# Kernel optimization log

Measured on AMD Instinct MI355X. Metric: run time of the kernel, lower is better.

## Reference

```python
import jax, jax.numpy as jnp
from jax import lax
import numpy as np

L, D, DM, E, DH, K, V, B, S = 4, 512, 128, 2, 128, 5, 50257, 2, 1024
EPS = 1e-6


def rmsnorm(x, w):
    return w * x * jax.lax.rsqrt(jnp.mean(x * x, axis=-1, keepdims=True) + EPS)


def rope(x):
    b, s, d = x.shape
    h = d // 2
    inv = 1.0 / (10000.0 ** (jnp.arange(h, dtype=jnp.float32) / h))
    freqs = jnp.arange(s, dtype=jnp.float32)[:, None] * inv[None, :]  # [S, h]
    emb = jnp.concatenate([freqs, freqs], axis=-1)  # [S, D]
    cos, sin = jnp.cos(emb)[None], jnp.sin(emb)[None]
    x1, x2 = x[..., :h], x[..., h:]
    rot = jnp.concatenate([-x2, x1], axis=-1)
    return x * cos + rot * sin


def causal_dwconv(x, w, b, dil):
    # x: [B,S,D]; w: [D,K] depthwise kernel; left-pad (K-1)*dil => causal.
    xc = jnp.transpose(x, (0, 2, 1))  # [B,D,S]
    k = w[:, None, :]  # [D,1,K]
    pad = (w.shape[-1] - 1) * dil
    y = lax.conv_general_dilated(xc, k, window_strides=(1,), padding=[(pad, 0)],
                                 rhs_dilation=(dil,),
                                 dimension_numbers=('NCH', 'OIH', 'NCH'),
                                 feature_group_count=x.shape[-1])
    return jnp.transpose(y, (0, 2, 1)) + b


def recurrence(x, win, bin_, wf, bf, wu, bu, wo, bo):
    # StructuredStateRecurrence: gated scan over time with memory dim DM.
    b_, s_, d_ = x.shape
    mu = jax.nn.silu(x @ win.T + bin_)            # [B,S,DM] silu(memory_proj_in)
    fx = x @ wf[:, :d_].T + bf                    # x-part of forget gate
    ux = x @ wu[:, :d_].T + bu                    # x-part of update gate
    ox = x @ wo[:, :d_].T + bo                    # x-part of output gate
    wfm, wum, wom = wf[:, d_:], wu[:, d_:], wo[:, d_:]

    def step(m, inp):
        fx_t, ux_t, mu_t, ox_t, x_t = inp
        f = jax.nn.sigmoid(fx_t + m @ wfm.T)
        u = jax.nn.sigmoid(ux_t + m @ wum.T)
        m = f * m + u * mu_t
        out = x_t + ox_t + m @ wom.T
        return m, out

    m0 = jnp.zeros((b_, DM), x.dtype)
    tr = lambda a: jnp.transpose(a, (1, 0, 2))
    m_final, ys = lax.scan(step, m0, (tr(fx), tr(ux), tr(mu), tr(ox), tr(x)))
    return jnp.transpose(ys, (1, 0, 2)), m_final


def setup_inputs() -> dict:
    key = jax.random.key(0)
    ks = iter(jax.random.split(key, 40))
    p = lambda shape, s=0.02: jax.random.normal(next(ks), shape, jnp.float32) * s
    return dict(
        tokens=jax.random.randint(next(ks), (B, S), 0, V),
        embed=p((V, D)),
        norm_w=jnp.ones((L, D)),
        dw_w=p((L, D, K), 0.1), dw_b=jnp.zeros((L, D)),
        pw_w=p((L, D, D)), pw_b=jnp.zeros((L, D)),
        rin_w=p((L, DM, D)), rin_b=jnp.zeros((L, DM)),
        rf_w=p((L, DM, D + DM)), rf_b=jnp.ones((L, DM)),
        ru_w=p((L, DM, D + DM)), ru_b=jnp.zeros((L, DM)),
        ro_w=p((L, D, D + DM)), ro_b=jnp.zeros((L, D)),
        rt_w=p((L, E, D)), rt_b=jnp.zeros((L, E)),
        e1_w=p((L, E, D, D)), e1_b=jnp.zeros((L, E, D)),
        e2_w=p((L, E, D, D)), e2_b=jnp.zeros((L, E, D)),
        fn_w=jnp.ones((L, D)),
        fd_w=p((L, DH, D)), fd_b=jnp.zeros((L, DH)),
        fu_w=p((L, D, DH)), fu_b=jnp.zeros((L, D)),
        final_norm_w=jnp.ones((D,)),
    )


def reference(tokens, embed, norm_w, dw_w, dw_b, pw_w, pw_b,
              rin_w, rin_b, rf_w, rf_b, ru_w, ru_b, ro_w, ro_b,
              rt_w, rt_b, e1_w, e1_b, e2_w, e2_b, fn_w,
              fd_w, fd_b, fu_w, fu_b, final_norm_w):
    dils = [max(1, int(np.exp(i * np.log(8) / L))) for i in range(L)]  # [1,1,2,4]
    x = embed[tokens]            # [B,S,D] token embedding
    x = rope(x)                  # rotary positional embedding (applied to full dim)
    for i in range(L):
        residual = x
        xn = rmsnorm(x, norm_w[i])
        # depthwise causal dilated conv + 1x1 pointwise conv
        xc = causal_dwconv(xn, dw_w[i], dw_b[i], dils[i])
        xc = xc @ pw_w[i].T + pw_b[i]
        # gated recurrent memory scan
        xr, _ = recurrence(xn, rin_w[i], rin_b[i], rf_w[i], rf_b[i],
                           ru_w[i], ru_b[i], ro_w[i], ro_b[i])
        h = xc + xr
        # EnhancedGatedFusion: softmax router over 2 dense experts
        r = jax.nn.softmax(h @ rt_w[i].T + rt_b[i], axis=-1)          # [B,S,E]
        hh = jax.nn.silu(jnp.einsum('bsd,eod->bseo', h, e1_w[i]) + e1_b[i])
        eo = jnp.einsum('bseo,epo->bsep', hh, e2_w[i]) + e2_b[i]      # [B,S,E,D]
        h = rmsnorm(h + jnp.einsum('bse,bsep->bsp', r, eo), fn_w[i])
        # LowRankFF: down -> GELU(exact) -> up
        h = h + (jax.nn.gelu(h @ fd_w[i].T + fd_b[i], approximate=False) @ fu_w[i].T + fu_b[i])
        x = h + residual
    x = rmsnorm(x, final_norm_w)
    logits = x @ embed.T          # tied output projection
    return logits
```

## Files before the change

### kernel.cpp

```cpp
#include <hip/hip_runtime.h>
#include <hip/hip_bf16.h>

#define Bsz 2
#define Ssz 1024
#define Dsz 512
#define DMs 128
#define Vsz 50257
#define ROWS (Bsz*Ssz)

typedef __attribute__((ext_vector_type(8))) short short8;
typedef __attribute__((ext_vector_type(4))) float f32x4;
typedef __attribute__((ext_vector_type(8))) int int8v;
typedef __attribute__((ext_vector_type(4))) int int4v;

#define DEV static __device__ __forceinline__

DEV unsigned short f2bf(float f){
  unsigned int u = __float_as_uint(f);
  unsigned int r = ((u >> 16) & 1u) + 0x7fffu;
  return (unsigned short)((u + r) >> 16);
}

__global__ __launch_bounds__(256) void k_embed_rope(
    const int* __restrict__ tokens, const float* __restrict__ embed, float* __restrict__ x)
{
  int row = blockIdx.x;
  int s = row & (Ssz-1);
  int t = threadIdx.x;
  int tok = tokens[row];
  const float* e = embed + (size_t)tok * Dsz;
  float e1 = e[t], e2 = e[t + 256];
  float inv = powf(10000.f, -(float)t * (1.f/256.f));
  float fr = (float)s * inv;
  float sn, cs;
  sincosf(fr, &sn, &cs);
  float* o = x + (size_t)row * Dsz;
  o[t]       = e1 * cs - e2 * sn;
  o[t + 256] = e2 * cs + e1 * sn;
}

__global__ __launch_bounds__(256) void k_rmsnorm(
    const float* __restrict__ a, const float* __restrict__ w, float* __restrict__ out)
{
  int row = blockIdx.x; int t = threadIdx.x;
  size_t base = (size_t)row * Dsz;
  float v0 = a[base + t];
  float v1 = a[base + t + 256];
  float ss = v0*v0 + v1*v1;
  #pragma unroll
  for (int off = 32; off > 0; off >>= 1) ss += __shfl_down(ss, off);
  __shared__ float sred[4];
  __shared__ float sscale;
  int wid = t >> 6, lane = t & 63;
  if (lane == 0) sred[wid] = ss;
  __syncthreads();
  if (t == 0) {
    float tot = sred[0] + sred[1] + sred[2] + sred[3];
    sscale = rsqrtf(tot * (1.f/Dsz) + 1e-6f);
  }
  __syncthreads();
  float sc = sscale;
  out[base + t]       = w[t]       * v0 * sc;
  out[base + t + 256] = w[t + 256] * v1 * sc;
}

__global__ __launch_bounds__(256) void k_rmsnorm_b16(
    const float* __restrict__ a, const float* __restrict__ w, unsigned short* __restrict__ out)
{
  int row = blockIdx.x; int t = threadIdx.x;
  size_t base = (size_t)row * Dsz;
  float v0 = a[base + t];
  float v1 = a[base + t + 256];
  float ss = v0*v0 + v1*v1;
  #pragma unroll
  for (int off = 32; off > 0; off >>= 1) ss += __shfl_down(ss, off);
  __shared__ float sred[4];
  __shared__ float sscale;
  int wid = t >> 6, lane = t & 63;
  if (lane == 0) sred[wid] = ss;
  __syncthreads();
  if (t == 0) {
    float tot = sred[0] + sred[1] + sred[2] + sred[3];
    sscale = rsqrtf(tot * (1.f/Dsz) + 1e-6f);
  }
  __syncthreads();
  float sc = sscale;
  out[base + t]       = f2bf(w[t]       * v0 * sc);
  out[base + t + 256] = f2bf(w[t + 256] * v1 * sc);
}

__global__ __launch_bounds__(256) void k_combine_norm(
    const float* __restrict__ h, const float* __restrict__ e0,
    const float* __restrict__ e1, const float* __restrict__ rg,
    const float* __restrict__ w, float* __restrict__ out)
{
  int row = blockIdx.x; int t = threadIdx.x;
  size_t base = (size_t)row * Dsz;
  float r0 = rg[row*2], r1 = rg[row*2+1];
  float v0 = h[base + t]       + r0*e0[base + t]       + r1*e1[base + t];
  float v1 = h[base + t + 256] + r0*e0[base + t + 256] + r1*e1[base + t + 256];
  float ss = v0*v0 + v1*v1;
  #pragma unroll
  for (int off = 32; off > 0; off >>= 1) ss += __shfl_down(ss, off);
  __shared__ float sred[4];
  __shared__ float sscale;
  int wid = t >> 6, lane = t & 63;
  if (lane == 0) sred[wid] = ss;
  __syncthreads();
  if (t == 0) {
    float tot = sred[0] + sred[1] + sred[2] + sred[3];
    sscale = rsqrtf(tot * (1.f/Dsz) + 1e-6f);
  }
  __syncthreads();
  float sc = sscale;
  out[base + t]       = w[t]       * v0 * sc;
  out[base + t + 256] = w[t + 256] * v1 * sc;
}

__global__ __launch_bounds__(256) void k_dwconv(
    const float* __restrict__ xn, const float* __restrict__ w,
    const float* __restrict__ bias, float* __restrict__ out, int dil)
{
  int row = blockIdx.x;
  int b = row >> 10, s = row & (Ssz-1);
  int t = threadIdx.x;
  #pragma unroll
  for (int dd = 0; dd < 2; ++dd) {
    int d = t + dd*256;
    float acc = bias[d];
    #pragma unroll
    for (int j = 0; j < 5; ++j) {
      int sp = s - (4 - j) * dil;
      if (sp >= 0) acc += w[d*5 + j] * xn[((size_t)(b*Ssz + sp))*Dsz + d];
    }
    out[(size_t)row*Dsz + d] = acc;
  }
}

__global__ __launch_bounds__(256) void k_gemm128(
    const float* __restrict__ A, int lda,
    const float* __restrict__ B, int ldb,
    const float* __restrict__ bias,
    float* __restrict__ C, int ldc,
    int M, int N, int K)
{
  __shared__ __align__(16) unsigned short As[128][40];
  __shared__ __align__(16) unsigned short Bs[128][40];
  int t = threadIdx.x;
  int m0 = blockIdx.y * 128;
  int n0 = blockIdx.x * 128;
  int wid = t >> 6, lane = t & 63;
  int wr = wid >> 1, wc = wid & 1;
  f32x4 acc[4][4] = {};
  int tr = t >> 3;
  int tc = (t & 7) * 4;

  for (int k0 = 0; k0 < K; k0 += 32) {
    #pragma unroll
    for (int rr = 0; rr < 128; rr += 32) {
      int row = rr + tr;
      float4 av = *reinterpret_cast<const float4*>(A + (size_t)(m0 + row)*lda + k0 + tc);
      ushort4 ap; ap.x = f2bf(av.x); ap.y = f2bf(av.y); ap.z = f2bf(av.z); ap.w = f2bf(av.w);
      *reinterpret_cast<ushort4*>(&As[row][tc]) = ap;
      int bn = n0 + row;
      float4 bv = make_float4(0.f, 0.f, 0.f, 0.f);
      if (bn < N) bv = *reinterpret_cast<const float4*>(B + (size_t)bn*ldb + k0 + tc);
      ushort4 bp; bp.x = f2bf(bv.x); bp.y = f2bf(bv.y); bp.z = f2bf(bv.z); bp.w = f2bf(bv.w);
      *reinterpret_cast<ushort4*>(&Bs[row][tc]) = bp;
    }
    __syncthreads();
    int kc = (lane >> 4) * 8;
    int ra = lane & 15;
    short8 af[4], bf_[4];
    #pragma unroll
    for (int mt = 0; mt < 4; ++mt)
      af[mt] = *reinterpret_cast<const short8*>(&As[wr*64 + mt*16 + ra][kc]);
    #pragma unroll
    for (int nt = 0; nt < 4; ++nt)
      bf_[nt] = *reinterpret_cast<const short8*>(&Bs[wc*64 + nt*16 + ra][kc]);
    #pragma unroll
    for (int mt = 0; mt < 4; ++mt)
      #pragma unroll
      for (int nt = 0; nt < 4; ++nt)
        acc[mt][nt] = __builtin_amdgcn_mfma_f32_16x16x32_bf16(af[mt], bf_[nt], acc[mt][nt], 0, 0, 0);
    __syncthreads();
  }

  #pragma unroll
  for (int mt = 0; mt < 4; ++mt) {
    #pragma unroll
    for (int nt = 0; nt < 4; ++nt) {
      int n = n0 + wc*64 + nt*16 + (lane & 15);
      if (n >= N) continue;
      float bv = bias ? bias[n] : 0.f;
      #pragma unroll
      for (int j = 0; j < 4; ++j) {
        int m = m0 + wr*64 + mt*16 + (lane >> 4)*4 + j;
        C[(size_t)m*ldc + n] = acc[mt][nt][j] + bv;
      }
    }
  }
}

template<int OP, int NADD>
DEV void gemm64_body(unsigned short (*As)[40], unsigned short (*Bs)[40],
                     const float* __restrict__ A, int lda,
                     const float* __restrict__ B, int ldb,
                     const float* __restrict__ bias,
                     float* __restrict__ C, int ldc,
                     int K, int m0, int n0, int t,
                     const float* __restrict__ add1,
                     const float* __restrict__ add2,
                     const float* __restrict__ add3)
{
  int lane = t & 63;
  int wid = t >> 6;
  int wr = wid >> 1, wc = wid & 1;
  f32x4 acc[2][2] = {};
  int srow = t >> 2;
  int scb  = (t & 3) * 8;

  const float* apg = A + (size_t)(m0 + srow)*lda + scb;
  const float* bpg = B + (size_t)(n0 + srow)*ldb + scb;

  for (int k0 = 0; k0 < K; k0 += 32) {
    float4 a0 = *reinterpret_cast<const float4*>(apg + k0);
    float4 a1 = *reinterpret_cast<const float4*>(apg + k0 + 4);
    float4 b0 = *reinterpret_cast<const float4*>(bpg + k0);
    float4 b1 = *reinterpret_cast<const float4*>(bpg + k0 + 4);
    short8 av, bv;
    av[0]=f2bf(a0.x); av[1]=f2bf(a0.y); av[2]=f2bf(a0.z); av[3]=f2bf(a0.w);
    av[4]=f2bf(a1.x); av[5]=f2bf(a1.y); av[6]=f2bf(a1.z); av[7]=f2bf(a1.w);
    bv[0]=f2bf(b0.x); bv[1]=f2bf(b0.y); bv[2]=f2bf(b0.z); bv[3]=f2bf(b0.w);
    bv[4]=f2bf(b1.x); bv[5]=f2bf(b1.y); bv[6]=f2bf(b1.z); bv[7]=f2bf(b1.w);
    *reinterpret_cast<short8*>(&As[srow][scb]) = av;
    *reinterpret_cast<short8*>(&Bs[srow][scb]) = bv;
    __syncthreads();
    int kc = (lane >> 4) * 8;
    int ra = lane & 15;
    short8 af[2], bf_[2];
    #pragma unroll
    for (int mt = 0; mt < 2; ++mt)
      af[mt] = *reinterpret_cast<const short8*>(&As[wr*32 + mt*16 + ra][kc]);
    #pragma unroll
    for (int nt = 0; nt < 2; ++nt)
      bf_[nt] = *reinterpret_cast<const short8*>(&Bs[wc*32 + nt*16 + ra][kc]);
    #pragma unroll
    for (int mt = 0; mt < 2; ++mt)
      #pragma unroll
      for (int nt = 0; nt < 2; ++nt)
        acc[mt][nt] = __builtin_amdgcn_mfma_f32_16x16x32_bf16(af[mt], bf_[nt], acc[mt][nt], 0, 0, 0);
    __syncthreads();
  }

  #pragma unroll
  for (int mt = 0; mt < 2; ++mt) {
    #pragma unroll
    for (int nt = 0; nt < 2; ++nt) {
      int n = n0 + wc*32 + nt*16 + (lane & 15);
      float bv = bias ? bias[n] : 0.f;
      #pragma unroll
      for (int j = 0; j < 4; ++j) {
        int m = m0 + wr*32 + mt*16 + (lane >> 4)*4 + j;
        float v = acc[mt][nt][j] + bv;
        if (OP == 1) v = v / (1.f + expf(-v));
        else if (OP == 2) v = 0.5f * v * (1.f + erff(v * 0.70710678118f));
        size_t idx = (size_t)m*ldc + n;
        if (NADD >= 1) v += add1[idx];
        if (NADD >= 2) v += add2[idx];
        if (NADD >= 3) v += add3[idx];
        C[idx] = v;
      }
    }
  }
}

template<int OP, int NADD>
__global__ __launch_bounds__(256) void k_gemm64(
    const float* __restrict__ A, int lda,
    const float* __restrict__ B, int ldb,
    const float* __restrict__ bias,
    float* __restrict__ C, int ldc, int K,
    const float* add1, const float* add2, const float* add3)
{
  __shared__ __align__(16) unsigned short As[64][40];
  __shared__ __align__(16) unsigned short Bs[64][40];
  gemm64_body<OP,NADD>(As, Bs, A, lda, B, ldb, bias, C, ldc, K,
                       blockIdx.y*64, blockIdx.x*64, threadIdx.x, add1, add2, add3);
}

__global__ __launch_bounds__(256) void k_proj3(
    const float* __restrict__ xn,
    const float* __restrict__ rin_w, const float* __restrict__ rin_b,
    const float* __restrict__ rf_w,  const float* __restrict__ rf_b,
    const float* __restrict__ ru_w,  const float* __restrict__ ru_b,
    float* __restrict__ mu, float* __restrict__ fx, float* __restrict__ ux)
{
  __shared__ __align__(16) unsigned short As[64][40];
  __shared__ __align__(16) unsigned short Bs[64][40];
  int which = blockIdx.x >> 1;
  int n0 = (blockIdx.x & 1) * 64;
  int m0 = blockIdx.y * 64;
  if (which == 0)
    gemm64_body<1,0>(As, Bs, xn, Dsz, rin_w, Dsz, rin_b, mu, DMs, Dsz, m0, n0, threadIdx.x, nullptr, nullptr, nullptr);
  else if (which == 1)
    gemm64_body<0,0>(As, Bs, xn, Dsz, rf_w, 640, rf_b, fx, DMs, Dsz, m0, n0, threadIdx.x, nullptr, nullptr, nullptr);
  else
    gemm64_body<0,0>(As, Bs, xn, Dsz, ru_w, 640, ru_b, ux, DMs, Dsz, m0, n0, threadIdx.x, nullptr, nullptr, nullptr);
}

template<int OP>
__global__ __launch_bounds__(256) void k_expair(
    const float* __restrict__ A0, const float* __restrict__ A1, int lda,
    const float* __restrict__ B0, const float* __restrict__ B1, int ldb,
    const float* __restrict__ bias0, const float* __restrict__ bias1,
    float* __restrict__ C0, float* __restrict__ C1, int ldc, int K)
{
  __shared__ __align__(16) unsigned short As[64][40];
  __shared__ __align__(16) unsigned short Bs[64][40];
  int e = blockIdx.x >> 3;
  int n0 = (blockIdx.x & 7) * 64;
  gemm64_body<OP,0>(As, Bs, e ? A1 : A0, lda, e ? B1 : B0, ldb,
                    e ? bias1 : bias0, e ? C1 : C0, ldc, K,
                    blockIdx.y*64, n0, threadIdx.x, nullptr, nullptr, nullptr);
}

__global__ __launch_bounds__(256) void k_f2b(
    const float* __restrict__ in, unsigned short* __restrict__ o, int n8)
{
  int stride = gridDim.x * 256;
  for (int i = blockIdx.x*256 + threadIdx.x; i < n8; i += stride) {
    float4 a = reinterpret_cast<const float4*>(in)[i*2];
    float4 b = reinterpret_cast<const float4*>(in)[i*2+1];
    short8 v;
    v[0]=f2bf(a.x); v[1]=f2bf(a.y); v[2]=f2bf(a.z); v[3]=f2bf(a.w);
    v[4]=f2bf(b.x); v[5]=f2bf(b.y); v[6]=f2bf(b.z); v[7]=f2bf(b.w);
    *reinterpret_cast<short8*>(o + (size_t)i*8) = v;
  }
}

__global__ __launch_bounds__(256) void k_gemm_logits(
    const unsigned short* __restrict__ A, const unsigned short* __restrict__ B,
    float* __restrict__ C, int M, int N, int K)
{
  __shared__ __align__(16) unsigned short As[128][40];
  __shared__ __align__(16) unsigned short Bs[128][40];
  int t = threadIdx.x;
  int lin = blockIdx.x + blockIdx.y * 16;
  int swz = (lin & 7) * 786 + (lin >> 3);
  int m0 = (swz & 15) * 128;
  int n0 = (swz >> 4) * 128;
  int wid = t >> 6, lane = t & 63;
  int wr = wid >> 1, wc = wid & 1;
  f32x4 acc[4][4] = {};
  int srow = t >> 1;
  int scb  = (t & 1) * 16;

  const unsigned short* ap = A + (size_t)(m0 + srow)*K + scb;
  int bn = n0 + srow; if (bn >= N) bn = N - 1;
  const unsigned short* bp = B + (size_t)bn*K + scb;

  for (int k0 = 0; k0 < K; k0 += 32) {
    short8 a0 = *reinterpret_cast<const short8*>(ap + k0);
    short8 a1 = *reinterpret_cast<const short8*>(ap + k0 + 8);
    short8 b0 = *reinterpret_cast<const short8*>(bp + k0);
    short8 b1 = *reinterpret_cast<const short8*>(bp + k0 + 8);
    *reinterpret_cast<short8*>(&As[srow][scb])     = a0;
    *reinterpret_cast<short8*>(&As[srow][scb + 8]) = a1;
    *reinterpret_cast<short8*>(&Bs[srow][scb])     = b0;
    *reinterpret_cast<short8*>(&Bs[srow][scb + 8]) = b1;
    __syncthreads();
    int kc = (lane >> 4) * 8;
    int ra = lane & 15;
    short8 af[4], bf_[4];
    #pragma unroll
    for (int mt = 0; mt < 4; ++mt)
      af[mt] = *reinterpret_cast<const short8*>(&As[wr*64 + mt*16 + ra][kc]);
    #pragma unroll
    for (int nt = 0; nt < 4; ++nt)
      bf_[nt] = *reinterpret_cast<const short8*>(&Bs[wc*64 + nt*16 + ra][kc]);
    #pragma unroll
    for (int mt = 0; mt < 4; ++mt)
      #pragma unroll
      for (int nt = 0; nt < 4; ++nt)
        acc[mt][nt] = __builtin_amdgcn_mfma_f32_16x16x32_bf16(af[mt], bf_[nt], acc[mt][nt], 0, 0, 0);
    __syncthreads();
  }

  #pragma unroll
  for (int mt = 0; mt < 4; ++mt) {
    #pragma unroll
    for (int nt = 0; nt < 4; ++nt) {
      int n = n0 + wc*64 + nt*16 + (lane & 15);
      if (n >= N) continue;
      #pragma unroll
      for (int j = 0; j < 4; ++j) {
        int m = m0 + wr*64 + mt*16 + (lane >> 4)*4 + j;
        C[(size_t)m*N + n] = acc[mt][nt][j];
      }
    }
  }
}

__global__ __launch_bounds__(256, 2) void k_scan_fused(
    const float* __restrict__ rf_w, const float* __restrict__ ru_w,
    const float* __restrict__ fx, const float* __restrict__ ux,
    const float* __restrict__ mu, float* __restrict__ Mout,
    const float* __restrict__ g1A, const float* __restrict__ g1B, int g1ldb,
    const float* __restrict__ g1bias, float* __restrict__ g1C,
    const float* __restrict__ g2A, const float* __restrict__ g2B, int g2ldb,
    const float* __restrict__ g2bias, float* __restrict__ g2C)
{
  __shared__ __align__(16) unsigned short As[64][40];
  __shared__ __align__(16) unsigned short Bs[64][40];
  __shared__ __align__(16) unsigned char mf8[2][DMs];

  if (blockIdx.x >= 2) {
    int bid = blockIdx.x - 2;
    int which = bid >> 8;
    int idx = bid & 255;
    int n0 = (idx & 7) * 64;
    int m0 = (idx >> 3) * 64;
    if (which == 0)
      gemm64_body<0,0>(As, Bs, g1A, Dsz, g1B, g1ldb, g1bias, g1C, Dsz, Dsz, m0, n0, threadIdx.x, nullptr, nullptr, nullptr);
    else
      gemm64_body<0,0>(As, Bs, g2A, Dsz, g2B, g2ldb, g2bias, g2C, Dsz, Dsz, m0, n0, threadIdx.x, nullptr, nullptr, nullptr);
    return;
  }

  __builtin_amdgcn_s_setprio(1);

  int b = blockIdx.x;
  int t = threadIdx.x;
  int l = t & 63;
  int w = t >> 6;
  int g = l >> 4;
  int i16 = l & 15;

  int8v w8[4];
  #pragma unroll
  for (int rt = 0; rt < 4; ++rt) {
    const float* src = (rt < 2 ? rf_w : ru_w) + (size_t)(w*32 + (rt&1)*16 + i16)*640 + 512 + g*32;
    int8v v;
    #pragma unroll
    for (int bq = 0; bq < 8; ++bq) {
      float4 f4 = *reinterpret_cast<const float4*>(src + bq*4);
      int rr = 0;
      rr = __builtin_amdgcn_cvt_pk_fp8_f32(f4.x, f4.y, rr, false);
      rr = __builtin_amdgcn_cvt_pk_fp8_f32(f4.z, f4.w, rr, true);
      v[bq] = rr;
    }
    w8[rt] = v;
  }

  if (t < DMs) mf8[0][t] = 0;

  bool writer = (i16 & 4) == 0;
  int rho = ((i16 >> 3) << 4) + (g << 2) + (i16 & 3);
  int r = w*32 + rho;
  bool jb0 = (i16 & 1), jb1 = (i16 & 2), ab = (i16 & 8);

  const float* fxp = fx + (size_t)b*Ssz*DMs + r;
  const float* uxp = ux + (size_t)b*Ssz*DMs + r;
  const float* mup = mu + (size_t)b*Ssz*DMs + r;
  float* mo = Mout + (size_t)b*Ssz*DMs + r;
  float mreg = 0.f, fxv = 0.f, uxv = 0.f, muv = 0.f;
  __syncthreads();
  if (writer) { fxv = fxp[0]; uxv = uxp[0]; muv = mup[0]; }

  const int SC = 0x7F7F7F7F;
  int cur = 0;
  for (int step = 0; step < Ssz; ++step) {
    int4v blo = *reinterpret_cast<const int4v*>(&mf8[cur][g*32]);
    int4v bhi = *reinterpret_cast<const int4v*>(&mf8[cur][g*32 + 16]);
    int8v bm;
    bm[0]=blo[0]; bm[1]=blo[1]; bm[2]=blo[2]; bm[3]=blo[3];
    bm[4]=bhi[0]; bm[5]=bhi[1]; bm[6]=bhi[2]; bm[7]=bhi[3];

    f32x4 zero = {0.f, 0.f, 0.f, 0.f};
    f32x4 a0 = __builtin_amdgcn_mfma_scale_f32_16x16x128_f8f6f4(w8[0], bm, zero, 0, 0, 0, SC, 0, SC);
    f32x4 a1 = __builtin_amdgcn_mfma_scale_f32_16x16x128_f8f6f4(w8[1], bm, zero, 0, 0, 0, SC, 0, SC);
    f32x4 a2 = __builtin_amdgcn_mfma_scale_f32_16x16x128_f8f6f4(w8[2], bm, zero, 0, 0, 0, SC, 0, SC);
    f32x4 a3 = __builtin_amdgcn_mfma_scale_f32_16x16x128_f8f6f4(w8[3], bm, zero, 0, 0, 0, SC, 0, SC);

    float f01 = jb0 ? a0[1] : a0[0];
    float f23 = jb0 ? a0[3] : a0[2];
    float fa0 = jb1 ? f23 : f01;
    float f01b = jb0 ? a1[1] : a1[0];
    float f23b = jb0 ? a1[3] : a1[2];
    float fa1 = jb1 ? f23b : f01b;
    float zf = ab ? fa1 : fa0;
    float u01 = jb0 ? a2[1] : a2[0];
    float u23 = jb0 ? a2[3] : a2[2];
    float ua0 = jb1 ? u23 : u01;
    float u01b = jb0 ? a3[1] : a3[0];
    float u23b = jb0 ? a3[3] : a3[2];
    float ua1 = jb1 ? u23b : u01b;
    float zu = ab ? ua1 : ua0;

    if (writer) {
      float f = __builtin_amdgcn_rcpf(1.f + __expf(-(zf + fxv)));
      float u = __builtin_amdgcn_rcpf(1.f + __expf(-(zu + uxv)));
      float mnew = f*mreg + u*muv;
      mreg = mnew;
      int p8 = __builtin_amdgcn_cvt_pk_fp8_f32(mnew, mnew, 0, false);
      mf8[cur^1][r] = (unsigned char)(p8 & 0xff);
      mo[(size_t)step*DMs] = mnew;
      if (step < Ssz-1) {
        fxv = fxp[(size_t)(step+1)*DMs];
        uxv = uxp[(size_t)(step+1)*DMs];
        muv = mup[(size_t)(step+1)*DMs];
      }
    }
    asm volatile("s_waitcnt lgkmcnt(0)\n\ts_barrier" ::: "memory");
    cur ^= 1;
  }
}

__global__ __launch_bounds__(64) void k_rt_softmax(
    const float* __restrict__ h, const float* __restrict__ rtw,
    const float* __restrict__ rtb, float* __restrict__ rg)
{
  int row = blockIdx.x; int lane = threadIdx.x;
  const float* hp = h + (size_t)row*Dsz;
  float a0 = 0.f, a1 = 0.f;
  #pragma unroll
  for (int k = lane; k < Dsz; k += 64) {
    float hv = hp[k];
    a0 += hv * rtw[k];
    a1 += hv * rtw[Dsz + k];
  }
  #pragma unroll
  for (int off = 32; off > 0; off >>= 1) {
    a0 += __shfl_down(a0, off);
    a1 += __shfl_down(a1, off);
  }
  if (lane == 0) {
    a0 += rtb[0]; a1 += rtb[1];
    float mx = fmaxf(a0, a1);
    float e0 = expf(a0 - mx), e1 = expf(a1 - mx);
    float s = e0 + e1;
    rg[row*2]     = e0 / s;
    rg[row*2 + 1] = e1 / s;
  }
}

extern "C" void kernel_launch(void* const* d_in, const int* in_sizes, int n_in,
                              void* d_out, int out_size, void* d_ws, size_t ws_size,
                              hipStream_t stream)
{
  const int*   tokens = (const int*)  d_in[0];
  const float* embed  = (const float*)d_in[1];
  const float* norm_w = (const float*)d_in[2];
  const float* dw_w   = (const float*)d_in[3];
  const float* dw_b   = (const float*)d_in[4];
  const float* pw_w   = (const float*)d_in[5];
  const float* pw_b   = (const float*)d_in[6];
  const float* rin_w  = (const float*)d_in[7];
  const float* rin_b  = (const float*)d_in[8];
  const float* rf_w   = (const float*)d_in[9];
  const float* rf_b   = (const float*)d_in[10];
  const float* ru_w   = (const float*)d_in[11];
  const float* ru_b   = (const float*)d_in[12];
  const float* ro_w   = (const float*)d_in[13];
  const float* ro_b   = (const float*)d_in[14];
  const float* rt_w   = (const float*)d_in[15];
  const float* rt_b   = (const float*)d_in[16];
  const float* e1_w   = (const float*)d_in[17];
  const float* e1_b   = (const float*)d_in[18];
  const float* e2_w   = (const float*)d_in[19];
  const float* e2_b   = (const float*)d_in[20];
  const float* fn_w   = (const float*)d_in[21];
  const float* fd_w   = (const float*)d_in[22];
  const float* fd_b   = (const float*)d_in[23];
  const float* fu_w   = (const float*)d_in[24];
  const float* fu_b   = (const float*)d_in[25];
  const float* fnorm  = (const float*)d_in[26];
  float* out = (float*)d_out;

  float* ws = (float*)d_ws;
  const size_t M1 = 1u << 20;
  float* x   = ws + 0*M1;
  float* xn  = ws + 1*M1;
  float* b2  = ws + 2*M1;
  float* b3  = ws + 3*M1;
  float* h   = ws + 4*M1;
  float* b5  = ws + 5*M1;
  float* b6  = ws + 6*M1;
  float* mu  = ws + 7*M1;
  float* fx  = ws + 7*M1 + 262144;
  float* ux  = ws + 7*M1 + 2*262144;
  float* Mb  = ws + 7*M1 + 3*262144;
  float* g   = ws + 8*M1;
  float* rg  = ws + 8*M1 + 262144;
  const size_t EMB_ELEMS = (size_t)Vsz * Dsz;
  unsigned short* embb = (unsigned short*)(ws + 9*M1);
  bool big = ws_size >= (size_t)(9*M1*4) + EMB_ELEMS*2 + 1024;

  const int dils[4] = {1, 1, 2, 4};

  k_embed_rope<<<ROWS, 256, 0, stream>>>(tokens, embed, x);

  for (int i = 0; i < 4; ++i) {
    k_rmsnorm<<<ROWS,256,0,stream>>>(x, norm_w + i*Dsz, xn);
    k_dwconv<<<ROWS,256,0,stream>>>(xn, dw_w + i*Dsz*5, dw_b + i*Dsz, b2, dils[i]);
    {
      dim3 gr(6, ROWS/64);
      k_proj3<<<gr,256,0,stream>>>(xn,
          rin_w + (size_t)i*DMs*Dsz, rin_b + i*DMs,
          rf_w  + (size_t)i*DMs*640, rf_b  + i*DMs,
          ru_w  + (size_t)i*DMs*640, ru_b  + i*DMs,
          mu, fx, ux);
    }
    k_scan_fused<<<2 + 512, 256, 0, stream>>>(
        rf_w + (size_t)i*DMs*640, ru_w + (size_t)i*DMs*640, fx, ux, mu, Mb,
        b2, pw_w + (size_t)i*Dsz*Dsz, Dsz, pw_b + i*Dsz, b3,
        xn, ro_w + (size_t)i*Dsz*640, 640, ro_b + i*Dsz, b5);
    {
      dim3 gr(Dsz/64, ROWS/64);
      k_gemm64<0,3><<<gr,256,0,stream>>>(Mb,DMs, ro_w + (size_t)i*Dsz*640 + 512,640, nullptr, h,Dsz, DMs, b3, xn, b5);
    }
    k_rt_softmax<<<ROWS,64,0,stream>>>(h, rt_w + i*2*Dsz, rt_b + i*2, rg);
    {
      dim3 ge(16, ROWS/64);
      k_expair<1><<<ge,256,0,stream>>>(h, h, Dsz,
          e1_w + (size_t)(i*2+0)*Dsz*Dsz, e1_w + (size_t)(i*2+1)*Dsz*Dsz, Dsz,
          e1_b + (i*2+0)*Dsz, e1_b + (i*2+1)*Dsz,
          b2, b5, Dsz, Dsz);
      k_expair<0><<<ge,256,0,stream>>>(b2, b5, Dsz,
          e2_w + (size_t)(i*2+0)*Dsz*Dsz, e2_w + (size_t)(i*2+1)*Dsz*Dsz, Dsz,
          e2_b + (i*2+0)*Dsz, e2_b + (i*2+1)*Dsz,
          b3, b6, Dsz, Dsz);
    }
    k_combine_norm<<<ROWS,256,0,stream>>>(h, b3, b6, rg, fn_w + i*Dsz, xn);
    {
      dim3 g1(DMs/64, ROWS/64), g2(Dsz/64, ROWS/64);
      k_gemm64<2,0><<<g1,256,0,stream>>>(xn,Dsz, fd_w + (size_t)i*DMs*Dsz,Dsz, fd_b + i*DMs, g,DMs, Dsz, nullptr,nullptr,nullptr);
      k_gemm64<0,2><<<g2,256,0,stream>>>(g,DMs, fu_w + (size_t)i*Dsz*DMs,DMs, fu_b + i*Dsz, x,Dsz, DMs, x, xn, nullptr);
    }
  }

  if (big) {
    unsigned short* xnb = (unsigned short*)b3;
    k_rmsnorm_b16<<<ROWS,256,0,stream>>>(x, fnorm, xnb);
    k_f2b<<<2048,256,0,stream>>>(embed, embb, (int)(EMB_ELEMS/8));
    dim3 grid(ROWS/128, (Vsz + 127)/128);
    k_gemm_logits<<<grid,256,0,stream>>>(xnb, embb, out, ROWS, Vsz, Dsz);
  } else {
    k_rmsnorm<<<ROWS,256,0,stream>>>(x, fnorm, xn);
    dim3 grid((Vsz + 127)/128, ROWS/128);
    k_gemm128<<<grid,256,0,stream>>>(xn,Dsz, embed,Dsz, nullptr, out,Vsz, ROWS,Vsz,Dsz);
  }
}
```

Baseline: 2.102 ms.

## Overlap embedding bf16 conversion with scan and load logits tiles via direct-to-LDS

The fp32-to-bf16 conversion of the embedding matrix moves out of its own launch before the logits GEMM and into extra blocks of the first layer's scan kernel. There it can run alongside the latency-bound sequential scan on otherwise idle CUs. The logits GEMM also switches its tile loads to global_load_lds direct-to-LDS transfers with an unpadded 32-wide LDS layout, which removes register staging. The unpadded layout may cause LDS bank conflicts on fragment reads, and the extra blocks may compete with the scan blocks for resources.

Result: slower. 2.150 ms (+2.3%).

```diff
diff --git a/kernel.cpp b/kernel.cpp
--- a/kernel.cpp
+++ b/kernel.cpp
@@ -19,6 +19,12 @@
   unsigned int u = __float_as_uint(f);
   unsigned int r = ((u >> 16) & 1u) + 0x7fffu;
   return (unsigned short)((u + r) >> 16);
+}
+
+DEV void gll16(const unsigned short* g, unsigned short* l) {
+  __builtin_amdgcn_global_load_lds(
+      (const __attribute__((address_space(1))) unsigned int*)(g),
+      (__attribute__((address_space(3))) unsigned int*)(l), 16, 0, 0);
 }
 
 __global__ __launch_bounds__(256) void k_embed_rope(
@@ -343,8 +349,8 @@
     const unsigned short* __restrict__ A, const unsigned short* __restrict__ B,
     float* __restrict__ C, int M, int N, int K)
 {
-  __shared__ __align__(16) unsigned short As[128][40];
-  __shared__ __align__(16) unsigned short Bs[128][40];
+  __shared__ __align__(16) unsigned short As[4096];
+  __shared__ __align__(16) unsigned short Bs[4096];
   int t = threadIdx.x;
   int lin = blockIdx.x + blockIdx.y * 16;
   int swz = (lin & 7) * 786 + (lin >> 3);
@@ -353,32 +359,38 @@
   int wid = t >> 6, lane = t & 63;
   int wr = wid >> 1, wc = wid & 1;
   f32x4 acc[4][4] = {};
-  int srow = t >> 1;
-  int scb  = (t & 1) * 16;
-
-  const unsigned short* ap = A + (size_t)(m0 + srow)*K + scb;
-  int bn = n0 + srow; if (bn >= N) bn = N - 1;
-  const unsigned short* bp = B + (size_t)bn*K + scb;
+
+  int row0 = t >> 2;
+  int kcb  = (t & 3) * 8;
+  int row1 = row0 + 64;
+  const unsigned short* a0p = A + (size_t)(m0 + row0)*K + kcb;
+  const unsigned short* a1p = A + (size_t)(m0 + row1)*K + kcb;
+  int bn0 = n0 + row0; if (bn0 >= N) bn0 = N - 1;
+  int bn1 = n0 + row1; if (bn1 >= N) bn1 = N - 1;
+  const unsigned short* b0p = B + (size_t)bn0*K + kcb;
+  const unsigned short* b1p = B + (size_t)bn1*K + kcb;
+
+  unsigned short* lA0 = As + wid*512;
+  unsigned short* lA1 = As + 2048 + wid*512;
+  unsigned short* lB0 = Bs + wid*512;
+  unsigned short* lB1 = Bs + 2048 + wid*512;
+
+  int kc = (lane >> 4) * 8;
+  int ra = lane & 15;
 
   for (int k0 = 0; k0 < K; k0 += 32) {
-    short8 a0 = *reinterpret_cast<const short8*>(ap + k0);
-    short8 a1 = *reinterpret_cast<const short8*>(ap + k0 + 8);
-    short8 b0 = *reinterpret_cast<const short8*>(bp + k0);
-    short8 b1 = *reinterpret_cast<const short8*>(bp + k0 + 8);
-    *reinterpret_cast<short8*>(&As[srow][scb])     = a0;
-    *reinterpret_cast<short8*>(&As[srow][scb + 8]) = a1;
-    *reinterpret_cast<short8*>(&Bs[srow][scb])     = b0;
-    *reinterpret_cast<short8*>(&Bs[srow][scb + 8]) = b1;
+    gll16(a0p + k0, lA0);
+    gll16(a1p + k0, lA1);
+    gll16(b0p + k0, lB0);
+    gll16(b1p + k0, lB1);
     __syncthreads();
-    int kc = (lane >> 4) * 8;
-    int ra = lane & 15;
     short8 af[4], bf_[4];
     #pragma unroll
     for (int mt = 0; mt < 4; ++mt)
-      af[mt] = *reinterpret_cast<const short8*>(&As[wr*64 + mt*16 + ra][kc]);
+      af[mt] = *reinterpret_cast<const short8*>(As + (wr*64 + mt*16 + ra)*32 + kc);
     #pragma unroll
     for (int nt = 0; nt < 4; ++nt)
-      bf_[nt] = *reinterpret_cast<const short8*>(&Bs[wc*64 + nt*16 + ra][kc]);
+      bf_[nt] = *reinterpret_cast<const short8*>(Bs + (wc*64 + nt*16 + ra)*32 + kc);
     #pragma unroll
     for (int mt = 0; mt < 4; ++mt)
       #pragma unroll
@@ -409,11 +421,26 @@
     const float* __restrict__ g1A, const float* __restrict__ g1B, int g1ldb,
     const float* __restrict__ g1bias, float* __restrict__ g1C,
     const float* __restrict__ g2A, const float* __restrict__ g2B, int g2ldb,
-    const float* __restrict__ g2bias, float* __restrict__ g2C)
+    const float* __restrict__ g2bias, float* __restrict__ g2C,
+    const float* __restrict__ f2bsrc, unsigned short* __restrict__ f2bdst, int f2bn8)
 {
   __shared__ __align__(16) unsigned short As[64][40];
   __shared__ __align__(16) unsigned short Bs[64][40];
   __shared__ __align__(16) unsigned char mf8[2][DMs];
+
+  if (blockIdx.x >= 514) {
+    int nb = gridDim.x - 514;
+    int stride = nb * 256;
+    for (int i = (blockIdx.x - 514)*256 + threadIdx.x; i < f2bn8; i += stride) {
+      float4 a = reinterpret_cast<const float4*>(f2bsrc)[i*2];
+      float4 b = reinterpret_cast<const float4*>(f2bsrc)[i*2+1];
+      short8 v;
+      v[0]=f2bf(a.x); v[1]=f2bf(a.y); v[2]=f2bf(a.z); v[3]=f2bf(a.w);
+      v[4]=f2bf(b.x); v[5]=f2bf(b.y); v[6]=f2bf(b.z); v[7]=f2bf(b.w);
+      *reinterpret_cast<short8*>(f2bdst + (size_t)i*8) = v;
+    }
+    return;
+  }
 
   if (blockIdx.x >= 2) {
     int bid = blockIdx.x - 2;
@@ -612,10 +639,16 @@
           ru_w  + (size_t)i*DMs*640, ru_b  + i*DMs,
           mu, fx, ux);
     }
-    k_scan_fused<<<2 + 512, 256, 0, stream>>>(
-        rf_w + (size_t)i*DMs*640, ru_w + (size_t)i*DMs*640, fx, ux, mu, Mb,
-        b2, pw_w + (size_t)i*Dsz*Dsz, Dsz, pw_b + i*Dsz, b3,
-        xn, ro_w + (size_t)i*Dsz*640, 640, ro_b + i*Dsz, b5);
+    {
+      bool fold = (i == 0) && big;
+      int nblk = 2 + 512 + (fold ? 2048 : 0);
+      k_scan_fused<<<nblk, 256, 0, stream>>>(
+          rf_w + (size_t)i*DMs*640, ru_w + (size_t)i*DMs*640, fx, ux, mu, Mb,
+          b2, pw_w + (size_t)i*Dsz*Dsz, Dsz, pw_b + i*Dsz, b3,
+          xn, ro_w + (size_t)i*Dsz*640, 640, ro_b + i*Dsz, b5,
+          fold ? embed : nullptr, fold ? embb : nullptr,
+          fold ? (int)(EMB_ELEMS/8) : 0);
+    }
     {
       dim3 gr(Dsz/64, ROWS/64);
       k_gemm64<0,3><<<gr,256,0,stream>>>(Mb,DMs, ro_w + (size_t)i*Dsz*640 + 512,640, nullptr, h,Dsz, DMs, b3, xn, b5);
@@ -643,7 +676,6 @@
   if (big) {
     unsigned short* xnb = (unsigned short*)b3;
     k_rmsnorm_b16<<<ROWS,256,0,stream>>>(x, fnorm, xnb);
-    k_f2b<<<2048,256,0,stream>>>(embed, embb, (int)(EMB_ELEMS/8));
     dim3 grid(ROWS/128, (Vsz + 127)/128);
     k_gemm_logits<<<grid,256,0,stream>>>(xnb, embb, out, ROWS, Vsz, Dsz);
   } else {
```
